# Kernel tuning notes

Measured on AMD Instinct MI355X. Metric: run time of the kernel, lower is better.

Reference implementation:

```python
import jax, jax.numpy as jnp
import numpy as np

N_HEAD = 12

def setup_inputs() -> dict:
    key = jax.random.key(0)
    ks = jax.random.split(key, 3)
    B, T, D = 4, 2048, 768
    x = jax.random.normal(ks[0], (B, T, D), dtype=jnp.float32)
    W_qkv = jax.random.normal(ks[1], (D, 3 * D), dtype=jnp.float32) * (1.0 / np.sqrt(D))
    b_qkv = jnp.zeros((3 * D,), dtype=jnp.float32)
    W_o = jax.random.normal(ks[2], (D, D), dtype=jnp.float32) * (1.0 / np.sqrt(D))
    b_o = jnp.zeros((D,), dtype=jnp.float32)
    return {"x": x, "W_qkv": W_qkv, "b_qkv": b_qkv, "W_o": W_o, "b_o": b_o}


def reference(x, W_qkv, b_qkv, W_o, b_o):
    B, T, D = x.shape
    H = N_HEAD
    hd = D // H
    qkv = x @ W_qkv + b_qkv                      # [B,T,3D]
    q, k, v = jnp.split(qkv, 3, axis=-1)
    # [B,T,D] -> [B,H,T,hd]
    q = q.reshape(B, T, H, hd).transpose(0, 2, 1, 3)
    k = k.reshape(B, T, H, hd).transpose(0, 2, 1, 3)
    v = v.reshape(B, T, H, hd).transpose(0, 2, 1, 3)
    scale = 1.0 / np.sqrt(hd).astype(np.float32)
    scores = jnp.einsum('bhqd,bhkd->bhqk', q, k) * scale   # [B,H,T,T]
    causal = jnp.tril(jnp.ones((T, T), dtype=bool))
    scores = jnp.where(causal[None, None, :, :], scores, -jnp.inf)
    attn = jax.nn.softmax(scores, axis=-1)
    out = jnp.einsum('bhqk,bhkd->bhqd', attn, v)            # [B,H,T,hd]
    out = out.transpose(0, 2, 1, 3).reshape(B, T, D)
    return out @ W_o + b_o
```

## Files before the change

### kernel.cpp

```cpp
#include <hip/hip_runtime.h>
#include <hip/hip_bf16.h>

typedef __bf16 bf16_t;
typedef float f32x4 __attribute__((ext_vector_type(4)));
typedef bf16_t bf16x8 __attribute__((ext_vector_type(8)));
typedef bf16_t bf16x4 __attribute__((ext_vector_type(4)));

#define MFMA16(a, b, c) __builtin_amdgcn_mfma_f32_16x16x32_bf16(a, b, c, 0, 0, 0)

#define QSCALE 0.18033688011112042f

__device__ __forceinline__ void gl_lds16(const bf16_t* g, bf16_t* l) {
    __builtin_amdgcn_global_load_lds(
        (const __attribute__((address_space(1))) unsigned int*)g,
        (__attribute__((address_space(3))) unsigned int*)l, 16, 0, 0);
}

__device__ __forceinline__ float fexp2(float x) {
    float y;
    asm("v_exp_f32 %0, %1" : "=v"(y) : "v"(x));
    return y;
}

__device__ __forceinline__ void conv_t_body(const float* __restrict__ in,
                                            bf16_t* __restrict__ out,
                                            int R, int C, int bx, int by,
                                            float (*t)[33]) {
    const int tx = threadIdx.x & 31;
    const int ty = threadIdx.x >> 5;
#pragma unroll
    for (int i = 0; i < 4; i++)
        t[ty + i * 8][tx] = in[(size_t)(by + ty + i * 8) * C + bx + tx];
    __syncthreads();
#pragma unroll
    for (int i = 0; i < 4; i++)
        out[(size_t)(bx + ty + i * 8) * R + by + tx] = (bf16_t)t[tx][ty + i * 8];
}

__global__ __launch_bounds__(256) void prep_k(
    const float* __restrict__ x,    bf16_t* __restrict__ xb,
    const float* __restrict__ Wqkv, bf16_t* __restrict__ Wt,
    const float* __restrict__ Wo,   bf16_t* __restrict__ Wot)
{
    __shared__ float t[32][33];
    const int blk = blockIdx.x;
    if (blk < 6144) {
        const int i = (blk * 256 + threadIdx.x) * 4;
        float4 v = *(const float4*)(x + i);
        bf16x4 o = { (bf16_t)v.x, (bf16_t)v.y, (bf16_t)v.z, (bf16_t)v.w };
        *(bf16x4*)(xb + i) = o;
    } else if (blk < 7872) {
        const int idx = blk - 6144;
        conv_t_body(Wqkv, Wt, 768, 2304, (idx % 72) * 32, (idx / 72) * 32, t);
    } else {
        const int idx = blk - 7872;
        conv_t_body(Wo, Wot, 768, 768, (idx % 24) * 32, (idx / 24) * 32, t);
    }
}

__global__ __launch_bounds__(256) void vtrans(const bf16_t* __restrict__ Vp,
                                              bf16_t* __restrict__ Vt) {
    __shared__ __align__(16) bf16_t Ts[64 * 72];
    const int t0 = blockIdx.x * 64;
    const int bh = blockIdx.y;
    const int r  = threadIdx.x >> 2;
    const int cb = (threadIdx.x & 3) * 16;
    const bf16_t* src = Vp + (((size_t)bh * 2048 + t0 + r) << 6) + cb;
    *(bf16x8*)(Ts + r * 72 + cb)     = *(const bf16x8*)(src);
    *(bf16x8*)(Ts + r * 72 + cb + 8) = *(const bf16x8*)(src + 8);
    __syncthreads();
    const int f  = threadIdx.x >> 2;
    const int tb = (threadIdx.x & 3) * 16;
    bf16_t* dst = Vt + (((size_t)bh * 64 + f) << 11) + t0 + tb;
    bf16x8 a, b;
#pragma unroll
    for (int i = 0; i < 8; i++) a[i] = Ts[(tb + i) * 72 + f];
#pragma unroll
    for (int i = 0; i < 8; i++) b[i] = Ts[(tb + 8 + i) * 72 + f];
    *(bf16x8*)(dst)     = a;
    *(bf16x8*)(dst + 8) = b;
}

template <int EPI>
__global__ __launch_bounds__(256) void gemm_bt(
    const bf16_t* __restrict__ A, const bf16_t* __restrict__ Bt,
    const float* __restrict__ bias,
    void* __restrict__ O0v, bf16_t* __restrict__ O1, bf16_t* __restrict__ O2,
    int M, int N, int K)
{
    __shared__ __align__(16) bf16_t As[2][128 * 32];
    __shared__ __align__(16) bf16_t Bs[2][128 * 32];

    const int tid  = threadIdx.x;
    const int wid  = tid >> 6;
    const int lane = tid & 63;
    const int quad = lane >> 4;
    const int l15  = lane & 15;
    const int wm   = (wid >> 1) * 64;
    const int wn   = (wid & 1) * 64;
    const int qs8  = (quad ^ ((l15 >> 1) & 3)) * 8;

    const int mtiles = M >> 7;
    const int mtpx   = mtiles >> 3;
    const int bid    = blockIdx.x;
    const int xcd    = bid & 7;
    const int slot   = bid >> 3;
    const int m0     = (xcd * mtpx + (slot % mtpx)) << 7;
    const int n0     = (slot / mtpx) << 7;

    f32x4 acc[4][4];
#pragma unroll
    for (int i = 0; i < 4; i++)
#pragma unroll
        for (int j = 0; j < 4; j++) acc[i][j] = (f32x4){0.f, 0.f, 0.f, 0.f};

    const int srow = tid >> 2;
    const int scol = (((tid & 3) ^ ((srow >> 1) & 3)) ) * 8;
    const bf16_t* ag0 = A  + (size_t)(m0 + srow) * K + scol;
    const bf16_t* ag1 = A  + (size_t)(m0 + 64 + srow) * K + scol;
    const bf16_t* bg0 = Bt + (size_t)(n0 + srow) * K + scol;
    const bf16_t* bg1 = Bt + (size_t)(n0 + 64 + srow) * K + scol;

    auto prefetch = [&](int k0, int buf) {
        gl_lds16(ag0 + k0, As[buf] + tid * 8);
        gl_lds16(ag1 + k0, As[buf] + 2048 + tid * 8);
        gl_lds16(bg0 + k0, Bs[buf] + tid * 8);
        gl_lds16(bg1 + k0, Bs[buf] + 2048 + tid * 8);
    };

    const int niter = K >> 5;
    prefetch(0, 0);
    for (int i = 0; i < niter; i++) {
        __syncthreads();
        if (i + 1 < niter) prefetch((i + 1) << 5, (i + 1) & 1);
        const bf16_t* Ap = As[i & 1];
        const bf16_t* Bp = Bs[i & 1];

        bf16x8 af[4], bfr[4];
#pragma unroll
        for (int ii = 0; ii < 4; ii++)
            af[ii] = *(const bf16x8*)(Ap + (wm + ii * 16 + l15) * 32 + qs8);
#pragma unroll
        for (int j = 0; j < 4; j++)
            bfr[j] = *(const bf16x8*)(Bp + (wn + j * 16 + l15) * 32 + qs8);
#pragma unroll
        for (int ii = 0; ii < 4; ii++)
#pragma unroll
            for (int j = 0; j < 4; j++)
                acc[ii][j] = MFMA16(af[ii], bfr[j], acc[ii][j]);
    }

    if (EPI == 0) {
        const int sec = n0 / 768;
        const float scale = (sec == 0) ? QSCALE : 1.f;
        bf16_t* dst = (sec == 0) ? (bf16_t*)O0v : (sec == 1 ? O1 : O2);
#pragma unroll
        for (int i = 0; i < 4; i++) {
            const int mbase = m0 + wm + i * 16 + quad * 4;
#pragma unroll
            for (int j = 0; j < 4; j++) {
                const int n  = n0 + wn + j * 16 + l15;
                const float bv = bias[n];
                const int d    = n - sec * 768;
                const int h    = d >> 6;
                const int feat = d & 63;
#pragma unroll
                for (int r = 0; r < 4; r++) {
                    const int mm = mbase + r;
                    const int b  = mm >> 11;
                    const int tt = mm & 2047;
                    const int bh = b * 12 + h;
                    dst[(((size_t)bh * 2048 + tt) << 6) + feat] =
                        (bf16_t)((acc[i][j][r] + bv) * scale);
                }
            }
        }
    } else {
#pragma unroll
        for (int i = 0; i < 4; i++) {
            const int mbase = m0 + wm + i * 16 + quad * 4;
#pragma unroll
            for (int j = 0; j < 4; j++) {
                const int n  = n0 + wn + j * 16 + l15;
                const float bv = bias[n];
#pragma unroll
                for (int r = 0; r < 4; r++)
                    ((float*)O0v)[(size_t)(mbase + r) * N + n] = acc[i][j][r] + bv;
            }
        }
    }
}

__global__ __launch_bounds__(256) void attn_k(
    const bf16_t* __restrict__ Q, const bf16_t* __restrict__ Kb,
    const bf16_t* __restrict__ Vt, bf16_t* __restrict__ AO)
{
    __shared__ __align__(16) bf16_t Ks[2 * 4096];
    __shared__ __align__(16) bf16_t Vs[2 * 4096];
    __shared__ __align__(16) bf16_t Ps[4 * 16 * 64];

    const int tid  = threadIdx.x;
    const int wid  = tid >> 6;
    const int lane = tid & 63;
    const int quad = lane >> 4;
    const int l15  = lane & 15;
    const int qs8  = (quad ^ ((l15 >> 1) & 3)) * 8;

    const int bid  = blockIdx.x;
    const int xcd  = bid & 7;
    const int slot = bid >> 3;
    const int bh   = xcd * 6 + (slot >> 4);
    const int p    = slot & 15;

    const bf16_t* Qb  = Q  + ((size_t)bh << 17);
    const bf16_t* Kbh = Kb + ((size_t)bh << 17);
    const bf16_t* Vbh = Vt + ((size_t)bh << 17);

    bf16_t* Pw = Ps + wid * 1024;
    const int swl = l15 & 7;
    bf16_t* pwr[4];
#pragma unroll
    for (int c = 0; c < 4; c++)
        pwr[c] = Pw + l15 * 64 + (((((c << 1) | (quad >> 1))) ^ swl) << 3) + ((quad & 1) << 2);
    const bf16_t* prd[2];
#pragma unroll
    for (int kk = 0; kk < 2; kk++)
        prd[kk] = Pw + l15 * 64 + ((((kk << 2) | quad) ^ swl) << 3);

    const bf16x8 ones = { (bf16_t)1.f, (bf16_t)1.f, (bf16_t)1.f, (bf16_t)1.f,
                          (bf16_t)1.f, (bf16_t)1.f, (bf16_t)1.f, (bf16_t)1.f };

    const int srow = tid >> 2;
    const int scol = (((tid & 3) ^ ((srow >> 1) & 3))) * 8;

    auto prefetch = [&](int j, int buf) {
        const int kv0 = j * 64;
        bf16_t* kd = Ks + buf * 4096 + tid * 8;
        bf16_t* vd = Vs + buf * 4096 + tid * 8;
#pragma unroll
        for (int c = 0; c < 2; c++) {
            gl_lds16(Kbh + (size_t)(kv0 + srow) * 64 + c * 32 + scol, kd + c * 2048);
            gl_lds16(Vbh + (size_t)srow * 2048 + kv0 + c * 32 + scol, vd + c * 2048);
        }
    };

    const int b = bh / 12;
    const int h = bh - b * 12;

#pragma unroll
    for (int half = 0; half < 2; half++) {
        const int qt = half == 0 ? (31 - p) : p;
        const int q0 = qt * 64;
        const int qg = q0 + wid * 16 + l15;

        bf16x8 qf[2];
        {
            const bf16_t* qp = Qb + ((size_t)qg << 6) + quad * 8;
            qf[0] = *(const bf16x8*)(qp);
            qf[1] = *(const bf16x8*)(qp + 32);
        }

        f32x4 lacc = (f32x4){0.f, 0.f, 0.f, 0.f};
        f32x4 oacc[4];
#pragma unroll
        for (int f = 0; f < 4; f++) oacc[f] = (f32x4){0.f, 0.f, 0.f, 0.f};

        const int cnt = qt + 1;
        prefetch(0, 0);

        for (int i = 0; i < cnt; i++) {
            __syncthreads();
            if (i + 1 < cnt) prefetch(i + 1, (i + 1) & 1);
            const bf16_t* Kp = Ks + (i & 1) * 4096;
            const bf16_t* Vp = Vs + (i & 1) * 4096;

            f32x4 st[4];
#pragma unroll
            for (int c = 0; c < 4; c++) {
                st[c] = (f32x4){0.f, 0.f, 0.f, 0.f};
#pragma unroll
                for (int kk = 0; kk < 2; kk++) {
                    bf16x8 kf = *(const bf16x8*)(Kp + kk * 2048 + (c * 16 + l15) * 32 + qs8);
                    st[c] = MFMA16(kf, qf[kk], st[c]);
                }
            }

            if (i == qt) {
                const int kvb = q0 + quad * 4;
#pragma unroll
                for (int c = 0; c < 4; c++)
#pragma unroll
                    for (int r = 0; r < 4; r++)
                        if (kvb + c * 16 + r > qg) st[c][r] = -3e38f;
            }

#pragma unroll
            for (int c = 0; c < 4; c++) {
                bf16x4 pk = { (bf16_t)fexp2(st[c][0]), (bf16_t)fexp2(st[c][1]),
                              (bf16_t)fexp2(st[c][2]), (bf16_t)fexp2(st[c][3]) };
                *(bf16x4*)pwr[c] = pk;
            }

            bf16x8 pb[2];
#pragma unroll
            for (int kk = 0; kk < 2; kk++)
                pb[kk] = *(const bf16x8*)prd[kk];

            lacc = MFMA16(ones, pb[0], lacc);
            lacc = MFMA16(ones, pb[1], lacc);

#pragma unroll
            for (int f = 0; f < 4; f++)
#pragma unroll
                for (int kk = 0; kk < 2; kk++) {
                    bf16x8 vf = *(const bf16x8*)(Vp + kk * 2048 + (f * 16 + l15) * 32 + qs8);
                    oacc[f] = MFMA16(vf, pb[kk], oacc[f]);
                }
        }
        __syncthreads();

        const float inv = 1.0f / lacc[0];
        bf16_t* dst = AO + ((size_t)(b * 2048 + qg)) * 768 + h * 64 + quad * 4;
#pragma unroll
        for (int f = 0; f < 4; f++) {
            bf16x4 o = { (bf16_t)(oacc[f][0] * inv), (bf16_t)(oacc[f][1] * inv),
                         (bf16_t)(oacc[f][2] * inv), (bf16_t)(oacc[f][3] * inv) };
            *(bf16x4*)(dst + f * 16) = o;
        }
    }
}

extern "C" void kernel_launch(void* const* d_in, const int* in_sizes, int n_in,
                              void* d_out, int out_size, void* d_ws, size_t ws_size,
                              hipStream_t stream)
{
    const float* x    = (const float*)d_in[0];
    const float* Wqkv = (const float*)d_in[1];
    const float* bqkv = (const float*)d_in[2];
    const float* Wo   = (const float*)d_in[3];
    const float* bo   = (const float*)d_in[4];
    float* out = (float*)d_out;

    const size_t per = (size_t)48 * 2048 * 64;
    bf16_t* Qs  = (bf16_t*)d_ws;
    bf16_t* Kk  = Qs + per;
    bf16_t* Vt  = Kk + per;
    bf16_t* AO  = Vt + per;
    bf16_t* xb  = AO + per;
    bf16_t* Wt  = xb + per;
    bf16_t* Wot = Wt + (size_t)2304 * 768;
    bf16_t* Vpl = (bf16_t*)d_out;

    prep_k<<<8448, 256, 0, stream>>>(x, xb, Wqkv, Wt, Wo, Wot);

    gemm_bt<0><<<18 * 64, 256, 0, stream>>>(
        xb, Wt, bqkv, (void*)Qs, Kk, Vpl, 8192, 2304, 768);
    vtrans<<<dim3(32, 48), 256, 0, stream>>>(Vpl, Vt);
    attn_k<<<768, 256, 0, stream>>>(Qs, Kk, Vt, AO);
    gemm_bt<1><<<6 * 64, 256, 0, stream>>>(
        AO, Wot, bo, (void*)out, nullptr, nullptr, 8192, 768, 768);
}
```

Before: 199.8 us.

## Use 2-wave GEMM blocks and 128-row attention tiles with longest-first scheduling

The GEMM now runs 128-thread blocks in which each of two waves computes a 128x64 tile, reusing the A fragments across 8x4 MFMAs. This doubles the accumulator registers per wave. The attention kernel drops the paired 64-row half scheme. Each block now processes one 128-row query tile, with every wave handling 32 query rows in two groups that share the K/V fragments, and blocks are ordered largest-first. Waves skip KV tiles entirely beyond their causal range, but they still sync and prefetch, and load imbalance across blocks may rise.

```diff
diff --git a/kernel.cpp b/kernel.cpp
--- a/kernel.cpp
+++ b/kernel.cpp
@@ -82,7 +82,7 @@
 }
 
 template <int EPI>
-__global__ __launch_bounds__(256) void gemm_bt(
+__global__ __launch_bounds__(128, 2) void gemm_bt(
     const bf16_t* __restrict__ A, const bf16_t* __restrict__ Bt,
     const float* __restrict__ bias,
     void* __restrict__ O0v, bf16_t* __restrict__ O1, bf16_t* __restrict__ O2,
@@ -96,8 +96,7 @@
     const int lane = tid & 63;
     const int quad = lane >> 4;
     const int l15  = lane & 15;
-    const int wm   = (wid >> 1) * 64;
-    const int wn   = (wid & 1) * 64;
+    const int wn   = wid * 64;
     const int qs8  = (quad ^ ((l15 >> 1) & 3)) * 8;
 
     const int mtiles = M >> 7;
@@ -108,24 +107,23 @@
     const int m0     = (xcd * mtpx + (slot % mtpx)) << 7;
     const int n0     = (slot / mtpx) << 7;
 
-    f32x4 acc[4][4];
-#pragma unroll
-    for (int i = 0; i < 4; i++)
+    f32x4 acc[8][4];
+#pragma unroll
+    for (int i = 0; i < 8; i++)
 #pragma unroll
         for (int j = 0; j < 4; j++) acc[i][j] = (f32x4){0.f, 0.f, 0.f, 0.f};
 
     const int srow = tid >> 2;
-    const int scol = (((tid & 3) ^ ((srow >> 1) & 3)) ) * 8;
-    const bf16_t* ag0 = A  + (size_t)(m0 + srow) * K + scol;
-    const bf16_t* ag1 = A  + (size_t)(m0 + 64 + srow) * K + scol;
-    const bf16_t* bg0 = Bt + (size_t)(n0 + srow) * K + scol;
-    const bf16_t* bg1 = Bt + (size_t)(n0 + 64 + srow) * K + scol;
+    const int scol = (((tid & 3) ^ ((srow >> 1) & 3))) * 8;
 
     auto prefetch = [&](int k0, int buf) {
-        gl_lds16(ag0 + k0, As[buf] + tid * 8);
-        gl_lds16(ag1 + k0, As[buf] + 2048 + tid * 8);
-        gl_lds16(bg0 + k0, Bs[buf] + tid * 8);
-        gl_lds16(bg1 + k0, Bs[buf] + 2048 + tid * 8);
+#pragma unroll
+        for (int s = 0; s < 4; s++) {
+            gl_lds16(A  + (size_t)(m0 + s * 32 + srow) * K + k0 + scol,
+                     As[buf] + s * 1024 + tid * 8);
+            gl_lds16(Bt + (size_t)(n0 + s * 32 + srow) * K + k0 + scol,
+                     Bs[buf] + s * 1024 + tid * 8);
+        }
     };
 
     const int niter = K >> 5;
@@ -136,15 +134,15 @@
         const bf16_t* Ap = As[i & 1];
         const bf16_t* Bp = Bs[i & 1];
 
-        bf16x8 af[4], bfr[4];
-#pragma unroll
-        for (int ii = 0; ii < 4; ii++)
-            af[ii] = *(const bf16x8*)(Ap + (wm + ii * 16 + l15) * 32 + qs8);
+        bf16x8 af[8], bfr[4];
+#pragma unroll
+        for (int ii = 0; ii < 8; ii++)
+            af[ii] = *(const bf16x8*)(Ap + (ii * 16 + l15) * 32 + qs8);
 #pragma unroll
         for (int j = 0; j < 4; j++)
             bfr[j] = *(const bf16x8*)(Bp + (wn + j * 16 + l15) * 32 + qs8);
 #pragma unroll
-        for (int ii = 0; ii < 4; ii++)
+        for (int ii = 0; ii < 8; ii++)
 #pragma unroll
             for (int j = 0; j < 4; j++)
                 acc[ii][j] = MFMA16(af[ii], bfr[j], acc[ii][j]);
@@ -155,8 +153,8 @@
         const float scale = (sec == 0) ? QSCALE : 1.f;
         bf16_t* dst = (sec == 0) ? (bf16_t*)O0v : (sec == 1 ? O1 : O2);
 #pragma unroll
-        for (int i = 0; i < 4; i++) {
-            const int mbase = m0 + wm + i * 16 + quad * 4;
+        for (int ii = 0; ii < 8; ii++) {
+            const int mbase = m0 + ii * 16 + quad * 4;
 #pragma unroll
             for (int j = 0; j < 4; j++) {
                 const int n  = n0 + wn + j * 16 + l15;
@@ -171,21 +169,21 @@
                     const int tt = mm & 2047;
                     const int bh = b * 12 + h;
                     dst[(((size_t)bh * 2048 + tt) << 6) + feat] =
-                        (bf16_t)((acc[i][j][r] + bv) * scale);
+                        (bf16_t)((acc[ii][j][r] + bv) * scale);
                 }
             }
         }
     } else {
 #pragma unroll
-        for (int i = 0; i < 4; i++) {
-            const int mbase = m0 + wm + i * 16 + quad * 4;
+        for (int ii = 0; ii < 8; ii++) {
+            const int mbase = m0 + ii * 16 + quad * 4;
 #pragma unroll
             for (int j = 0; j < 4; j++) {
                 const int n  = n0 + wn + j * 16 + l15;
                 const float bv = bias[n];
 #pragma unroll
                 for (int r = 0; r < 4; r++)
-                    ((float*)O0v)[(size_t)(mbase + r) * N + n] = acc[i][j][r] + bv;
+                    ((float*)O0v)[(size_t)(mbase + r) * N + n] = acc[ii][j][r] + bv;
             }
         }
     }
@@ -197,7 +195,7 @@
 {
     __shared__ __align__(16) bf16_t Ks[2 * 4096];
     __shared__ __align__(16) bf16_t Vs[2 * 4096];
-    __shared__ __align__(16) bf16_t Ps[4 * 16 * 64];
+    __shared__ __align__(16) bf16_t Ps[4 * 2048];
 
     const int tid  = threadIdx.x;
     const int wid  = tid >> 6;
@@ -208,15 +206,16 @@
 
     const int bid  = blockIdx.x;
     const int xcd  = bid & 7;
-    const int slot = bid >> 3;
-    const int bh   = xcd * 6 + (slot >> 4);
-    const int p    = slot & 15;
+    const int rank = bid >> 3;
+    const int qi   = 15 - rank / 6;
+    const int bh   = xcd * 6 + (rank % 6);
+    const int q0   = qi << 7;
 
     const bf16_t* Qb  = Q  + ((size_t)bh << 17);
     const bf16_t* Kbh = Kb + ((size_t)bh << 17);
     const bf16_t* Vbh = Vt + ((size_t)bh << 17);
 
-    bf16_t* Pw = Ps + wid * 1024;
+    bf16_t* Pw = Ps + wid * 2048;
     const int swl = l15 & 7;
     bf16_t* pwr[4];
 #pragma unroll
@@ -247,84 +246,107 @@
     const int b = bh / 12;
     const int h = bh - b * 12;
 
-#pragma unroll
-    for (int half = 0; half < 2; half++) {
-        const int qt = half == 0 ? (31 - p) : p;
-        const int q0 = qt * 64;
-        const int qg = q0 + wid * 16 + l15;
-
-        bf16x8 qf[2];
-        {
-            const bf16_t* qp = Qb + ((size_t)qg << 6) + quad * 8;
-            qf[0] = *(const bf16x8*)(qp);
-            qf[1] = *(const bf16x8*)(qp + 32);
-        }
-
-        f32x4 lacc = (f32x4){0.f, 0.f, 0.f, 0.f};
-        f32x4 oacc[4];
-#pragma unroll
-        for (int f = 0; f < 4; f++) oacc[f] = (f32x4){0.f, 0.f, 0.f, 0.f};
-
-        const int cnt = qt + 1;
-        prefetch(0, 0);
-
-        for (int i = 0; i < cnt; i++) {
-            __syncthreads();
-            if (i + 1 < cnt) prefetch(i + 1, (i + 1) & 1);
-            const bf16_t* Kp = Ks + (i & 1) * 4096;
-            const bf16_t* Vp = Vs + (i & 1) * 4096;
-
-            f32x4 st[4];
+    const int qw0 = q0 + wid * 32;
+    const int qwave_max = qw0 + 31;
+
+    bf16x8 qf[2][2];
+#pragma unroll
+    for (int g = 0; g < 2; g++) {
+        const bf16_t* qp = Qb + ((size_t)(qw0 + g * 16 + l15) << 6) + quad * 8;
+        qf[g][0] = *(const bf16x8*)(qp);
+        qf[g][1] = *(const bf16x8*)(qp + 32);
+    }
+
+    f32x4 lacc[2];
+    f32x4 oacc[2][4];
+#pragma unroll
+    for (int g = 0; g < 2; g++) {
+        lacc[g] = (f32x4){0.f, 0.f, 0.f, 0.f};
+#pragma unroll
+        for (int f = 0; f < 4; f++) oacc[g][f] = (f32x4){0.f, 0.f, 0.f, 0.f};
+    }
+
+    const int cnt = 2 * qi + 2;
+    prefetch(0, 0);
+
+    for (int i = 0; i < cnt; i++) {
+        __syncthreads();
+        if (i + 1 < cnt) prefetch(i + 1, (i + 1) & 1);
+        const int kv0 = i * 64;
+        if (kv0 > qwave_max) continue;
+        const bf16_t* Kp = Ks + (i & 1) * 4096;
+        const bf16_t* Vp = Vs + (i & 1) * 4096;
+
+        f32x4 st[2][4];
+#pragma unroll
+        for (int c = 0; c < 4; c++) {
+            bf16x8 kf0 = *(const bf16x8*)(Kp + (c * 16 + l15) * 32 + qs8);
+            bf16x8 kf1 = *(const bf16x8*)(Kp + 2048 + (c * 16 + l15) * 32 + qs8);
+#pragma unroll
+            for (int g = 0; g < 2; g++) {
+                f32x4 z = (f32x4){0.f, 0.f, 0.f, 0.f};
+                z = MFMA16(kf0, qf[g][0], z);
+                st[g][c] = MFMA16(kf1, qf[g][1], z);
+            }
+        }
+
+        if (kv0 + 63 > qw0) {
+#pragma unroll
+            for (int g = 0; g < 2; g++) {
+                const int qg = qw0 + g * 16 + l15;
+#pragma unroll
+                for (int c = 0; c < 4; c++) {
+                    const int kvb = kv0 + c * 16 + quad * 4;
+#pragma unroll
+                    for (int r = 0; r < 4; r++)
+                        if (kvb + r > qg) st[g][c][r] = -3e38f;
+                }
+            }
+        }
+
+#pragma unroll
+        for (int g = 0; g < 2; g++)
 #pragma unroll
             for (int c = 0; c < 4; c++) {
-                st[c] = (f32x4){0.f, 0.f, 0.f, 0.f};
-#pragma unroll
-                for (int kk = 0; kk < 2; kk++) {
-                    bf16x8 kf = *(const bf16x8*)(Kp + kk * 2048 + (c * 16 + l15) * 32 + qs8);
-                    st[c] = MFMA16(kf, qf[kk], st[c]);
-                }
-            }
-
-            if (i == qt) {
-                const int kvb = q0 + quad * 4;
-#pragma unroll
-                for (int c = 0; c < 4; c++)
-#pragma unroll
-                    for (int r = 0; r < 4; r++)
-                        if (kvb + c * 16 + r > qg) st[c][r] = -3e38f;
-            }
-
-#pragma unroll
-            for (int c = 0; c < 4; c++) {
-                bf16x4 pk = { (bf16_t)fexp2(st[c][0]), (bf16_t)fexp2(st[c][1]),
-                              (bf16_t)fexp2(st[c][2]), (bf16_t)fexp2(st[c][3]) };
-                *(bf16x4*)pwr[c] = pk;
-            }
-
-            bf16x8 pb[2];
+                bf16x4 pk = { (bf16_t)fexp2(st[g][c][0]), (bf16_t)fexp2(st[g][c][1]),
+                              (bf16_t)fexp2(st[g][c][2]), (bf16_t)fexp2(st[g][c][3]) };
+                *(bf16x4*)(pwr[c] + g * 1024) = pk;
+            }
+
+        bf16x8 pb[2][2];
+#pragma unroll
+        for (int g = 0; g < 2; g++)
 #pragma unroll
             for (int kk = 0; kk < 2; kk++)
-                pb[kk] = *(const bf16x8*)prd[kk];
-
-            lacc = MFMA16(ones, pb[0], lacc);
-            lacc = MFMA16(ones, pb[1], lacc);
-
-#pragma unroll
-            for (int f = 0; f < 4; f++)
-#pragma unroll
-                for (int kk = 0; kk < 2; kk++) {
-                    bf16x8 vf = *(const bf16x8*)(Vp + kk * 2048 + (f * 16 + l15) * 32 + qs8);
-                    oacc[f] = MFMA16(vf, pb[kk], oacc[f]);
-                }
-        }
-        __syncthreads();
-
-        const float inv = 1.0f / lacc[0];
+                pb[g][kk] = *(const bf16x8*)(prd[kk] + g * 1024);
+
+#pragma unroll
+        for (int g = 0; g < 2; g++) {
+            lacc[g] = MFMA16(ones, pb[g][0], lacc[g]);
+            lacc[g] = MFMA16(ones, pb[g][1], lacc[g]);
+        }
+
+#pragma unroll
+        for (int f = 0; f < 4; f++) {
+            bf16x8 vf0 = *(const bf16x8*)(Vp + (f * 16 + l15) * 32 + qs8);
+            bf16x8 vf1 = *(const bf16x8*)(Vp + 2048 + (f * 16 + l15) * 32 + qs8);
+#pragma unroll
+            for (int g = 0; g < 2; g++) {
+                oacc[g][f] = MFMA16(vf0, pb[g][0], oacc[g][f]);
+                oacc[g][f] = MFMA16(vf1, pb[g][1], oacc[g][f]);
+            }
+        }
+    }
+
+#pragma unroll
+    for (int g = 0; g < 2; g++) {
+        const int qg = qw0 + g * 16 + l15;
+        const float inv = 1.0f / lacc[g][0];
         bf16_t* dst = AO + ((size_t)(b * 2048 + qg)) * 768 + h * 64 + quad * 4;
 #pragma unroll
         for (int f = 0; f < 4; f++) {
-            bf16x4 o = { (bf16_t)(oacc[f][0] * inv), (bf16_t)(oacc[f][1] * inv),
-                         (bf16_t)(oacc[f][2] * inv), (bf16_t)(oacc[f][3] * inv) };
+            bf16x4 o = { (bf16_t)(oacc[g][f][0] * inv), (bf16_t)(oacc[g][f][1] * inv),
+                         (bf16_t)(oacc[g][f][2] * inv), (bf16_t)(oacc[g][f][3] * inv) };
             *(bf16x4*)(dst + f * 16) = o;
         }
     }
@@ -353,10 +375,10 @@
 
     prep_k<<<8448, 256, 0, stream>>>(x, xb, Wqkv, Wt, Wo, Wot);
 
-    gemm_bt<0><<<18 * 64, 256, 0, stream>>>(
+    gemm_bt<0><<<18 * 64, 128, 0, stream>>>(
         xb, Wt, bqkv, (void*)Qs, Kk, Vpl, 8192, 2304, 768);
     vtrans<<<dim3(32, 48), 256, 0, stream>>>(Vpl, Vt);
     attn_k<<<768, 256, 0, stream>>>(Qs, Kk, Vt, AO);
-    gemm_bt<1><<<6 * 64, 256, 0, stream>>>(
+    gemm_bt<1><<<6 * 64, 128, 0, stream>>>(
         AO, Wot, bo, (void*)out, nullptr, nullptr, 8192, 768, 768);
 }
```

After: 215.0 us. 1.08x slower.
